# Kernel tuning notes

Hardware: AMD Instinct MI355X
Metric: run time of the kernel (lower is better)

The kernel has to match this reference:

```python
import jax, jax.numpy as jnp
import numpy as np

N_NODES = 131072
N_EDGES = 2097152
N_GRAPHS = 2048
IN_CH, HID, OUT = 12, 64, 4


def gcn_conv(x, W, b, src, dst, n_nodes):
    """PyG GCNConv: out = D^{-1/2} (A + I) D^{-1/2} (x W) + b.
    Degree computed at target nodes including self loops (edge_weight=1)."""
    h = x @ W  # [N, F_out]
    # degree with self loops: in-degree + 1
    deg = jax.ops.segment_sum(jnp.ones((src.shape[0],), x.dtype), dst,
                              num_segments=n_nodes) + 1.0
    dinv = jax.lax.rsqrt(deg)  # [N]
    norm = dinv[src] * dinv[dst]  # [E]
    # scatter-add messages from src to dst
    agg = jax.ops.segment_sum(h[src] * norm[:, None], dst, num_segments=n_nodes)
    # self-loop contribution: norm_ii = dinv[i]^2
    agg = agg + h * (dinv * dinv)[:, None]
    return agg + b


def global_mean_pool(x, batch, n_graphs):
    sums = jax.ops.segment_sum(x, batch, num_segments=n_graphs)
    cnt = jax.ops.segment_sum(jnp.ones((x.shape[0],), x.dtype), batch,
                              num_segments=n_graphs)
    return sums / jnp.maximum(cnt, 1.0)[:, None]


def setup_inputs() -> dict:
    key = jax.random.key(0)
    ks = jax.random.split(key, 9)
    x = jax.random.normal(ks[0], (N_NODES, IN_CH), dtype=jnp.float32)
    edge_index = jax.random.randint(ks[1], (2, N_EDGES), 0, N_NODES, dtype=jnp.int64)
    batch = jnp.sort(jax.random.randint(ks[2], (N_NODES,), 0, N_GRAPHS, dtype=jnp.int64))
    def glorot(k, shape):
        lim = np.sqrt(6.0 / (shape[0] + shape[1]))
        return jax.random.uniform(k, shape, jnp.float32, -lim, lim)
    return {
        "x": x,
        "edge_index": edge_index,
        "batch": batch,
        "W1": glorot(ks[3], (IN_CH, HID)),
        "b1": jnp.zeros((HID,), jnp.float32),
        "W2": glorot(ks[4], (HID, HID)),
        "b2": jnp.zeros((HID,), jnp.float32),
        "Wfc": glorot(ks[5], (HID, OUT)),
        "bfc": jnp.zeros((OUT,), jnp.float32),
    }


def reference(x, edge_index, batch, W1, b1, W2, b2, Wfc, bfc):
    src, dst = edge_index[0], edge_index[1]
    h = jax.nn.relu(gcn_conv(x, W1, b1, src, dst, N_NODES))
    h = jax.nn.relu(gcn_conv(h, W2, b2, src, dst, N_NODES))
    g = global_mean_pool(h, batch, N_GRAPHS)  # [n_graphs, HID]
    return jax.nn.sigmoid(g @ Wfc + bfc)  # [n_graphs, OUT]
```

## Files before the change

kernel.cpp:

```cpp
#include <hip/hip_runtime.h>
#include <hip/hip_bf16.h>


#define N_NODES 131072
#define N_EDGES 2097152
#define N_GRAPHS 2048
#define IN_CH 12
#define HID 64
#define OUT_CH 4
#define NBUCK 512
#define CHUNK 8192
#define STRIDE 4608
#define CSR_STRIDE 5120
#define CAP 5120

typedef float f32x2 __attribute__((ext_vector_type(2)));

__device__ __forceinline__ unsigned short f2bf(float f) {
    unsigned u = __float_as_uint(f);
    return (unsigned short)((u + 0x7fffu + ((u >> 16) & 1u)) >> 16);
}
__device__ __forceinline__ unsigned pack2bf(float lo, float hi) {
    return (unsigned)f2bf(lo) | ((unsigned)f2bf(hi) << 16);
}
__device__ __forceinline__ float bflo(unsigned v) { return __uint_as_float(v << 16); }
__device__ __forceinline__ float bfhi(unsigned v) { return __uint_as_float(v & 0xFFFF0000u); }

__global__ __launch_bounds__(1024, 4)
void bucket_kernel(const int* __restrict__ src, const int* __restrict__ dst,
                   int* __restrict__ bucket_count, int* __restrict__ staged) {
    __shared__ int hist[NBUCK];
    __shared__ int lscan[NBUCK];
    __shared__ int gbase[NBUCK];
    __shared__ int cursor[NBUCK];
    __shared__ int sorted[CHUNK];
    int tid = threadIdx.x;
    int base = blockIdx.x * CHUNK;
    if (tid < NBUCK) { hist[tid] = 0; cursor[tid] = 0; }
    __syncthreads();
    int d8[8], s8[8];
#pragma unroll
    for (int k = 0; k < 8; k++) {
        int i = base + k * 1024 + tid;
        d8[k] = dst[i];
        s8[k] = src[i];
        atomicAdd(&hist[d8[k] >> 8], 1);
    }
    __syncthreads();
    if (tid < NBUCK) lscan[tid] = hist[tid];
    __syncthreads();
    for (int off = 1; off < NBUCK; off <<= 1) {
        int u = (tid < NBUCK && tid >= off) ? lscan[tid - off] : 0;
        __syncthreads();
        if (tid < NBUCK) lscan[tid] += u;
        __syncthreads();
    }
    if (tid < NBUCK) gbase[tid] = atomicAdd(&bucket_count[tid], hist[tid]);
    __syncthreads();
#pragma unroll
    for (int k = 0; k < 8; k++) {
        int b = d8[k] >> 8;
        int start = lscan[b] - hist[b];
        int p = start + atomicAdd(&cursor[b], 1);
        sorted[p] = ((d8[k] & 255) << 17) | s8[k];
    }
    __syncthreads();
    int wid = tid >> 6, lane = tid & 63;
    int g16 = lane >> 4, k16 = lane & 15;
    for (int b0 = wid * 4; b0 < NBUCK; b0 += 64) {
        int b = b0 + g16;
        int cb = hist[b];
        int lbase = lscan[b] - cb;
        int gb = b * STRIDE + gbase[b];
        for (int k = k16; k < cb; k += 16) staged[gb + k] = sorted[lbase + k];
    }
}

__global__ void build_kernel(const int* __restrict__ bucket_count, const int* __restrict__ staged,
                             int2* __restrict__ rowbounds, float* __restrict__ dinv,
                             int* __restrict__ csr, const float* __restrict__ x,
                             unsigned short* __restrict__ xb) {
    __shared__ int sl[STRIDE];
    __shared__ int image[CAP];
    __shared__ int cnt[256];
    __shared__ int scn[256];
    __shared__ int loff[256];
    __shared__ int cursor[256];
    __shared__ int totalS;
    int b = blockIdx.x;
    int tid = threadIdx.x;
    int count = bucket_count[b];
    const int* st = staged + b * STRIDE;
    cnt[tid] = 0;
    cursor[tid] = 0;
    for (int i = tid; i < count; i += 256) sl[i] = st[i];
    __syncthreads();
    for (int i = tid; i < count; i += 256) atomicAdd(&cnt[(sl[i] >> 17) & 255], 1);
    __syncthreads();
    int deg = cnt[tid];
    int degp = (deg + 3) & ~3;
    scn[tid] = degp;
    __syncthreads();
    for (int off = 1; off < 256; off <<= 1) {
        int u = (tid >= off) ? scn[tid - off] : 0;
        __syncthreads();
        scn[tid] += u;
        __syncthreads();
    }
    int lo = scn[tid] - degp;
    loff[tid] = lo;
    int nbase = (b << 8) + tid;
    int gb = b * CSR_STRIDE;
    rowbounds[nbase] = make_int2(gb + lo, gb + lo + degp);
    float dv = rsqrtf((float)deg + 1.0f);
    dinv[nbase] = dv;
    if (tid == 255) totalS = lo + degp;
    {
        const float* xp = x + nbase * IN_CH;
        unsigned o[8];
#pragma unroll
        for (int k = 0; k < 6; k++) o[k] = pack2bf(dv * xp[2 * k], dv * xp[2 * k + 1]);
        o[6] = 0; o[7] = 0;
        uint4* dstp = (uint4*)(xb + nbase * 16);
        dstp[0] = make_uint4(o[0], o[1], o[2], o[3]);
        dstp[1] = make_uint4(o[4], o[5], o[6], o[7]);
    }
    if (b == 0 && tid < 2)
        ((uint4*)(xb + (size_t)N_NODES * 16))[tid] = make_uint4(0, 0, 0, 0);
    __syncthreads();
    for (int i = tid; i < count; i += 256) {
        int rec = sl[i];
        int s = rec & 0x1FFFF;
        int dq = (rec >> 17) & 255;
        int p = loff[dq] + atomicAdd(&cursor[dq], 1);
        int val = s << 6;
        if (p < CAP) image[p] = val;
        else csr[gb + p] = val;
    }
    __syncthreads();
    int padval = N_NODES << 6;
    for (int p = loff[tid] + deg; p < loff[tid] + degp; p++) {
        if (p < CAP) image[p] = padval;
        else csr[gb + p] = padval;
    }
    __syncthreads();
    int lim = totalS < CAP ? totalS : CAP;
    int* dstp = csr + gb;
    for (int i = tid; i < lim; i += 256) dstp[i] = image[i];
}

__global__ void agg_x_kernel(const int2* __restrict__ rowbounds, const int* __restrict__ csr,
                             const float* __restrict__ dinv,
                             const unsigned short* __restrict__ xb, float* __restrict__ aggx) {
    int tid = threadIdx.x;
    int w = tid >> 6, lane = tid & 63, sub = lane >> 1, p = lane & 1;
    int qoff = 8 * p;
    int node = (blockIdx.x * 4 + w) * 32 + sub;
    int2 rb = rowbounds[node];
    float dn = dinv[node];
    f32x2 a0[4] = {{0, 0}, {0, 0}, {0, 0}, {0, 0}};
    f32x2 a1[4] = {{0, 0}, {0, 0}, {0, 0}, {0, 0}};
    f32x2 a2[4] = {{0, 0}, {0, 0}, {0, 0}, {0, 0}};
    f32x2 a3[4] = {{0, 0}, {0, 0}, {0, 0}, {0, 0}};
    for (int j = rb.x; j < rb.y; j += 4) {
        int4 e = *(const int4*)(csr + j);
        uint4 u0 = *(const uint4*)(xb + (e.x >> 2) + qoff);
        uint4 u1 = *(const uint4*)(xb + (e.y >> 2) + qoff);
        uint4 u2 = *(const uint4*)(xb + (e.z >> 2) + qoff);
        uint4 u3 = *(const uint4*)(xb + (e.w >> 2) + qoff);
        a0[0] += (f32x2){bflo(u0.x), bfhi(u0.x)};
        a0[1] += (f32x2){bflo(u0.y), bfhi(u0.y)};
        a0[2] += (f32x2){bflo(u0.z), bfhi(u0.z)};
        a0[3] += (f32x2){bflo(u0.w), bfhi(u0.w)};
        a1[0] += (f32x2){bflo(u1.x), bfhi(u1.x)};
        a1[1] += (f32x2){bflo(u1.y), bfhi(u1.y)};
        a1[2] += (f32x2){bflo(u1.z), bfhi(u1.z)};
        a1[3] += (f32x2){bflo(u1.w), bfhi(u1.w)};
        a2[0] += (f32x2){bflo(u2.x), bfhi(u2.x)};
        a2[1] += (f32x2){bflo(u2.y), bfhi(u2.y)};
        a2[2] += (f32x2){bflo(u2.z), bfhi(u2.z)};
        a2[3] += (f32x2){bflo(u2.w), bfhi(u2.w)};
        a3[0] += (f32x2){bflo(u3.x), bfhi(u3.x)};
        a3[1] += (f32x2){bflo(u3.y), bfhi(u3.y)};
        a3[2] += (f32x2){bflo(u3.z), bfhi(u3.z)};
        a3[3] += (f32x2){bflo(u3.w), bfhi(u3.w)};
    }
    uint4 su = *(const uint4*)(xb + node * 16 + qoff);
    a0[0] += (f32x2){bflo(su.x), bfhi(su.x)};
    a0[1] += (f32x2){bflo(su.y), bfhi(su.y)};
    a0[2] += (f32x2){bflo(su.z), bfhi(su.z)};
    a0[3] += (f32x2){bflo(su.w), bfhi(su.w)};
    f32x2 nd = {dn, dn};
    f32x2 s0 = nd * ((a0[0] + a1[0]) + (a2[0] + a3[0]));
    f32x2 s1 = nd * ((a0[1] + a1[1]) + (a2[1] + a3[1]));
    f32x2 s2 = nd * ((a0[2] + a1[2]) + (a2[2] + a3[2]));
    f32x2 s3 = nd * ((a0[3] + a1[3]) + (a2[3] + a3[3]));
    float4 o0 = make_float4(s0[0], s0[1], s1[0], s1[1]);
    float4 o1 = make_float4(s2[0], s2[1], s3[0], s3[1]);
    *(float4*)(aggx + node * 16 + qoff) = o0;
    *(float4*)(aggx + node * 16 + qoff + 4) = o1;
}

__global__ void w1w2_kernel(const float* __restrict__ aggx, const float* __restrict__ W1,
                            const float* __restrict__ b1, const float* __restrict__ W2,
                            const float* __restrict__ dinv, unsigned int* __restrict__ hout) {
    __shared__ float sW1[IN_CH * HID];
    __shared__ float sW2[HID * HID];
    __shared__ float sA[64 * 17];
    __shared__ float sh1t[HID * 65];
    int tid = threadIdx.x;
    for (int i = tid; i < IN_CH * HID; i += 256) sW1[i] = W1[i];
    for (int i = tid; i < HID * HID; i += 256) sW2[i] = W2[i];
    int node0 = blockIdx.x * 64;
    {
        float4 v = *(const float4*)(aggx + node0 * 16 + tid * 4);
        int n = tid >> 2, part = (tid & 3) * 4;
        sA[n * 17 + part + 0] = v.x;
        sA[n * 17 + part + 1] = v.y;
        sA[n * 17 + part + 2] = v.z;
        sA[n * 17 + part + 3] = v.w;
    }
    __syncthreads();
    int w = tid >> 6, c = tid & 63;
    float bc = b1[c];
#pragma unroll
    for (int it = 0; it < 4; it++) {
        int n0 = w * 16 + it * 4;
        float a0 = bc, a1 = bc, a2 = bc, a3 = bc;
#pragma unroll
        for (int k = 0; k < IN_CH; k++) {
            float wv = sW1[k * HID + c];
            a0 += sA[(n0 + 0) * 17 + k] * wv;
            a1 += sA[(n0 + 1) * 17 + k] * wv;
            a2 += sA[(n0 + 2) * 17 + k] * wv;
            a3 += sA[(n0 + 3) * 17 + k] * wv;
        }
        float4 o = make_float4(fmaxf(a0, 0.0f), fmaxf(a1, 0.0f),
                               fmaxf(a2, 0.0f), fmaxf(a3, 0.0f));
        *(float4*)&sh1t[c * 65 + n0] = o;
    }
    __syncthreads();
    int nq = tid >> 4, c4 = (tid & 15) * 4;
    float4 a0 = {0, 0, 0, 0}, a1 = {0, 0, 0, 0}, a2 = {0, 0, 0, 0}, a3 = {0, 0, 0, 0};
#pragma unroll 4
    for (int k = 0; k < HID; k++) {
        float4 wv = *(const float4*)&sW2[k * HID + c4];
        float4 hv = *(const float4*)&sh1t[k * 65 + nq * 4];
        a0.x += hv.x * wv.x; a0.y += hv.x * wv.y; a0.z += hv.x * wv.z; a0.w += hv.x * wv.w;
        a1.x += hv.y * wv.x; a1.y += hv.y * wv.y; a1.z += hv.y * wv.z; a1.w += hv.y * wv.w;
        a2.x += hv.z * wv.x; a2.y += hv.z * wv.y; a2.z += hv.z * wv.z; a2.w += hv.z * wv.w;
        a3.x += hv.w * wv.x; a3.y += hv.w * wv.y; a3.z += hv.w * wv.z; a3.w += hv.w * wv.w;
    }
    int nb = node0 + nq * 4;
    float dv0 = dinv[nb + 0], dv1 = dinv[nb + 1], dv2 = dinv[nb + 2], dv3 = dinv[nb + 3];
    unsigned int p0 = (unsigned int)__builtin_amdgcn_cvt_pk_fp8_f32(dv0 * a0.x, dv0 * a0.y, 0, false);
    p0 = (unsigned int)__builtin_amdgcn_cvt_pk_fp8_f32(dv0 * a0.z, dv0 * a0.w, (int)p0, true);
    unsigned int p1 = (unsigned int)__builtin_amdgcn_cvt_pk_fp8_f32(dv1 * a1.x, dv1 * a1.y, 0, false);
    p1 = (unsigned int)__builtin_amdgcn_cvt_pk_fp8_f32(dv1 * a1.z, dv1 * a1.w, (int)p1, true);
    unsigned int p2 = (unsigned int)__builtin_amdgcn_cvt_pk_fp8_f32(dv2 * a2.x, dv2 * a2.y, 0, false);
    p2 = (unsigned int)__builtin_amdgcn_cvt_pk_fp8_f32(dv2 * a2.z, dv2 * a2.w, (int)p2, true);
    unsigned int p3 = (unsigned int)__builtin_amdgcn_cvt_pk_fp8_f32(dv3 * a3.x, dv3 * a3.y, 0, false);
    p3 = (unsigned int)__builtin_amdgcn_cvt_pk_fp8_f32(dv3 * a3.z, dv3 * a3.w, (int)p3, true);
    int cl = c4 >> 2;
    hout[(nb + 0) * 16 + cl] = p0;
    hout[(nb + 1) * 16 + cl] = p1;
    hout[(nb + 2) * 16 + cl] = p2;
    hout[(nb + 3) * 16 + cl] = p3;
    if (blockIdx.x == 0 && tid < 16)
        hout[(size_t)N_NODES * 16 + tid] = 0;
}

__device__ __forceinline__ void add_fp8(f32x2* a, uint2 u) {
    a[0] += __builtin_amdgcn_cvt_pk_f32_fp8((int)u.x, false);
    a[1] += __builtin_amdgcn_cvt_pk_f32_fp8((int)u.x, true);
    a[2] += __builtin_amdgcn_cvt_pk_f32_fp8((int)u.y, false);
    a[3] += __builtin_amdgcn_cvt_pk_f32_fp8((int)u.y, true);
}

__device__ __forceinline__ void agg_body(int beg, int end, const int* __restrict__ csr,
                                         const unsigned char* __restrict__ h,
                                         int qoff, float* r) {
    f32x2 a0[4] = {{0, 0}, {0, 0}, {0, 0}, {0, 0}};
    f32x2 a1[4] = {{0, 0}, {0, 0}, {0, 0}, {0, 0}};
    f32x2 a2[4] = {{0, 0}, {0, 0}, {0, 0}, {0, 0}};
    f32x2 a3[4] = {{0, 0}, {0, 0}, {0, 0}, {0, 0}};
    int j = beg;
    for (; j + 8 <= end; j += 8) {
        int4 ea = *(const int4*)(csr + j);
        int4 eb = *(const int4*)(csr + j + 4);
        uint2 u0 = *(const uint2*)(h + ea.x + qoff);
        uint2 u1 = *(const uint2*)(h + ea.y + qoff);
        uint2 u2 = *(const uint2*)(h + ea.z + qoff);
        uint2 u3 = *(const uint2*)(h + ea.w + qoff);
        uint2 u4 = *(const uint2*)(h + eb.x + qoff);
        uint2 u5 = *(const uint2*)(h + eb.y + qoff);
        uint2 u6 = *(const uint2*)(h + eb.z + qoff);
        uint2 u7 = *(const uint2*)(h + eb.w + qoff);
        add_fp8(a0, u0); add_fp8(a1, u1); add_fp8(a2, u2); add_fp8(a3, u3);
        add_fp8(a0, u4); add_fp8(a1, u5); add_fp8(a2, u6); add_fp8(a3, u7);
    }
    if (j < end) {
        int4 ea = *(const int4*)(csr + j);
        uint2 u0 = *(const uint2*)(h + ea.x + qoff);
        uint2 u1 = *(const uint2*)(h + ea.y + qoff);
        uint2 u2 = *(const uint2*)(h + ea.z + qoff);
        uint2 u3 = *(const uint2*)(h + ea.w + qoff);
        add_fp8(a0, u0); add_fp8(a1, u1); add_fp8(a2, u2); add_fp8(a3, u3);
    }
#pragma unroll
    for (int k = 0; k < 4; k++) {
        f32x2 s = (a0[k] + a1[k]) + (a2[k] + a3[k]);
        r[2 * k] = s[0];
        r[2 * k + 1] = s[1];
    }
}

__global__ void agg_pool_kernel(const int2* __restrict__ rowbounds, const int* __restrict__ csr,
                                const float* __restrict__ dinv,
                                const unsigned char* __restrict__ h,
                                const float* __restrict__ b, const int* __restrict__ batch,
                                float* __restrict__ pool, float* __restrict__ gcnt) {
    __shared__ float red[32][HID];
    __shared__ int gids[32];
    int tid = threadIdx.x;
    int w = tid >> 6, lane = tid & 63, sub = lane >> 3, q = lane & 7;
    int qoff = 8 * q;
    int node = (blockIdx.x * 4 + w) * 8 + sub;
    int2 rb = rowbounds[node];
    float dn = dinv[node];
    float r[8];
    agg_body(rb.x, rb.y, csr, h, qoff, r);
    uint2 su = *(const uint2*)(h + node * HID + qoff);
    f32x2 s0 = __builtin_amdgcn_cvt_pk_f32_fp8((int)su.x, false);
    f32x2 s1 = __builtin_amdgcn_cvt_pk_f32_fp8((int)su.x, true);
    f32x2 s2 = __builtin_amdgcn_cvt_pk_f32_fp8((int)su.y, false);
    f32x2 s3 = __builtin_amdgcn_cvt_pk_f32_fp8((int)su.y, true);
    float4 b0 = *(const float4*)&b[qoff];
    float4 b1 = *(const float4*)&b[qoff + 4];
    float4 v0, v1;
    v0.x = fmaxf(dn * (r[0] + s0[0]) + b0.x, 0.0f);
    v0.y = fmaxf(dn * (r[1] + s0[1]) + b0.y, 0.0f);
    v0.z = fmaxf(dn * (r[2] + s1[0]) + b0.z, 0.0f);
    v0.w = fmaxf(dn * (r[3] + s1[1]) + b0.w, 0.0f);
    v1.x = fmaxf(dn * (r[4] + s2[0]) + b1.x, 0.0f);
    v1.y = fmaxf(dn * (r[5] + s2[1]) + b1.y, 0.0f);
    v1.z = fmaxf(dn * (r[6] + s3[0]) + b1.z, 0.0f);
    v1.w = fmaxf(dn * (r[7] + s3[1]) + b1.w, 0.0f);
    int nl = w * 8 + sub;
    *(float4*)&red[nl][qoff] = v0;
    *(float4*)&red[nl][qoff + 4] = v1;
    if (q == 0) gids[nl] = batch[node];
    __syncthreads();
    if (tid < 64) {
        int c = tid;
        float acc = 0.0f;
        int cur = gids[0], cnt = 0;
        for (int n = 0; n < 32; n++) {
            int g = gids[n];
            if (g != cur) {
                atomicAdd(&pool[cur * HID + c], acc);
                if (c == 0) atomicAdd(&gcnt[cur], (float)cnt);
                acc = 0.0f; cnt = 0; cur = g;
            }
            acc += red[n][c];
            cnt++;
        }
        atomicAdd(&pool[cur * HID + c], acc);
        if (c == 0) atomicAdd(&gcnt[cur], (float)cnt);
    }
}

__global__ void final_kernel(const float* __restrict__ pool, const float* __restrict__ gcnt,
                             const float* __restrict__ Wfc, const float* __restrict__ bfc,
                             float* __restrict__ out) {
    int idx = blockIdx.x * 256 + threadIdx.x;
    if (idx >= N_GRAPHS * OUT_CH) return;
    int g = idx >> 2, o = idx & 3;
    float inv = 1.0f / fmaxf(gcnt[g], 1.0f);
    float acc = bfc[o];
#pragma unroll
    for (int k = 0; k < HID; k++) acc += pool[g * HID + k] * inv * Wfc[k * OUT_CH + o];
    out[idx] = 1.0f / (1.0f + expf(-acc));
}

extern "C" void kernel_launch(void* const* d_in, const int* in_sizes, int n_in,
                              void* d_out, int out_size, void* d_ws, size_t ws_size,
                              hipStream_t stream) {
    const float* x   = (const float*)d_in[0];
    const int* eidx  = (const int*)d_in[1];
    const int* batch = (const int*)d_in[2];
    const float* W1  = (const float*)d_in[3];
    const float* b1  = (const float*)d_in[4];
    const float* W2  = (const float*)d_in[5];
    const float* b2  = (const float*)d_in[6];
    const float* Wfc = (const float*)d_in[7];
    const float* bfc = (const float*)d_in[8];
    float* out = (float*)d_out;

    const int* src = eidx;
    const int* dst = eidx + N_EDGES;

    unsigned char* hB = (unsigned char*)d_ws;
    int*   csr    = (int*)(hB + (size_t)(N_NODES + 1) * HID);
    int*   staged = csr + (size_t)NBUCK * CSR_STRIDE;
    float* dinv   = (float*)(staged + (size_t)NBUCK * STRIDE);
    int2*  rowbounds = (int2*)(dinv + N_NODES);
    int*   bucket_count = (int*)(rowbounds + N_NODES);
    float* pool   = (float*)(bucket_count + NBUCK);
    float* gcnt   = pool + N_GRAPHS * HID;
    unsigned short* xb = (unsigned short*)(gcnt + N_GRAPHS);
    float* aggx   = (float*)(xb + (size_t)(N_NODES + 1) * 16);

    hipMemsetAsync(bucket_count, 0, (size_t)NBUCK * 4, stream);
    hipMemsetAsync(pool, 0, (size_t)(N_GRAPHS * HID + N_GRAPHS) * 4, stream);

    bucket_kernel<<<N_EDGES / CHUNK, 1024, 0, stream>>>(src, dst, bucket_count, staged);
    build_kernel<<<NBUCK, 256, 0, stream>>>(bucket_count, staged, rowbounds, dinv, csr, x, xb);

    agg_x_kernel<<<N_NODES / 128, 256, 0, stream>>>(rowbounds, csr, dinv, xb, aggx);
    w1w2_kernel<<<N_NODES / 64, 256, 0, stream>>>(aggx, W1, b1, W2, dinv, (unsigned int*)hB);

    agg_pool_kernel<<<N_NODES / 32, 256, 0, stream>>>(rowbounds, csr, dinv, hB, b2, batch,
                                                      pool, gcnt);

    final_kernel<<<(N_GRAPHS * OUT_CH + 255) / 256, 256, 0, stream>>>(pool, gcnt, Wfc, bfc, out);
}
```

Measured before the change: 190.3 us.

## Replace bucketed two-pass CSR build with atomic count, reserve, and place

Replaces the shared-memory bucket sort and per-bucket build with three kernels. The first counts in-degrees with global atomics and records each edge's rank in a byte array. The second scans degrees per block and reserves CSR space with a global atomic cursor. The third scatters each edge directly to its slot. This removes the staging buffer and the LDS sort, but adds global atomics on random addresses, scattered CSR writes, and a rank stored in 8 bits that wraps if any node has in-degree of 256 or more. Row placement now depends on the order in which blocks reach the atomic cursor, so edge order inside a row is also nondeterministic.

```diff
diff --git a/kernel.cpp b/kernel.cpp
--- a/kernel.cpp
+++ b/kernel.cpp
@@ -8,11 +8,7 @@
 #define IN_CH 12
 #define HID 64
 #define OUT_CH 4
-#define NBUCK 512
-#define CHUNK 8192
-#define STRIDE 4608
-#define CSR_STRIDE 5120
-#define CAP 5120
+#define CSR_CAP 2560000
 
 typedef float f32x2 __attribute__((ext_vector_type(2)));
 
@@ -26,79 +22,28 @@
 __device__ __forceinline__ float bflo(unsigned v) { return __uint_as_float(v << 16); }
 __device__ __forceinline__ float bfhi(unsigned v) { return __uint_as_float(v & 0xFFFF0000u); }
 
-__global__ __launch_bounds__(1024, 4)
-void bucket_kernel(const int* __restrict__ src, const int* __restrict__ dst,
-                   int* __restrict__ bucket_count, int* __restrict__ staged) {
-    __shared__ int hist[NBUCK];
-    __shared__ int lscan[NBUCK];
-    __shared__ int gbase[NBUCK];
-    __shared__ int cursor[NBUCK];
-    __shared__ int sorted[CHUNK];
-    int tid = threadIdx.x;
-    int base = blockIdx.x * CHUNK;
-    if (tid < NBUCK) { hist[tid] = 0; cursor[tid] = 0; }
-    __syncthreads();
-    int d8[8], s8[8];
-#pragma unroll
-    for (int k = 0; k < 8; k++) {
-        int i = base + k * 1024 + tid;
-        d8[k] = dst[i];
-        s8[k] = src[i];
-        atomicAdd(&hist[d8[k] >> 8], 1);
-    }
-    __syncthreads();
-    if (tid < NBUCK) lscan[tid] = hist[tid];
-    __syncthreads();
-    for (int off = 1; off < NBUCK; off <<= 1) {
-        int u = (tid < NBUCK && tid >= off) ? lscan[tid - off] : 0;
-        __syncthreads();
-        if (tid < NBUCK) lscan[tid] += u;
-        __syncthreads();
-    }
-    if (tid < NBUCK) gbase[tid] = atomicAdd(&bucket_count[tid], hist[tid]);
-    __syncthreads();
-#pragma unroll
-    for (int k = 0; k < 8; k++) {
-        int b = d8[k] >> 8;
-        int start = lscan[b] - hist[b];
-        int p = start + atomicAdd(&cursor[b], 1);
-        sorted[p] = ((d8[k] & 255) << 17) | s8[k];
-    }
-    __syncthreads();
-    int wid = tid >> 6, lane = tid & 63;
-    int g16 = lane >> 4, k16 = lane & 15;
-    for (int b0 = wid * 4; b0 < NBUCK; b0 += 64) {
-        int b = b0 + g16;
-        int cb = hist[b];
-        int lbase = lscan[b] - cb;
-        int gb = b * STRIDE + gbase[b];
-        for (int k = k16; k < cb; k += 16) staged[gb + k] = sorted[lbase + k];
-    }
-}
-
-__global__ void build_kernel(const int* __restrict__ bucket_count, const int* __restrict__ staged,
-                             int2* __restrict__ rowbounds, float* __restrict__ dinv,
-                             int* __restrict__ csr, const float* __restrict__ x,
-                             unsigned short* __restrict__ xb) {
-    __shared__ int sl[STRIDE];
-    __shared__ int image[CAP];
-    __shared__ int cnt[256];
+__global__ void count_kernel(const int* __restrict__ dst, int* __restrict__ deg,
+                             unsigned char* __restrict__ rank) {
+    int i = (blockIdx.x * 256 + threadIdx.x) * 4;
+    int4 d = *(const int4*)(dst + i);
+    unsigned r0 = (unsigned)atomicAdd(&deg[d.x], 1);
+    unsigned r1 = (unsigned)atomicAdd(&deg[d.y], 1);
+    unsigned r2 = (unsigned)atomicAdd(&deg[d.z], 1);
+    unsigned r3 = (unsigned)atomicAdd(&deg[d.w], 1);
+    *(uchar4*)(rank + i) = make_uchar4((unsigned char)r0, (unsigned char)r1,
+                                       (unsigned char)r2, (unsigned char)r3);
+}
+
+__global__ void reserve_kernel(const int* __restrict__ deg, int* __restrict__ gcur,
+                               int2* __restrict__ rowbounds, float* __restrict__ dinv,
+                               int* __restrict__ csr, const float* __restrict__ x,
+                               unsigned short* __restrict__ xb) {
     __shared__ int scn[256];
-    __shared__ int loff[256];
-    __shared__ int cursor[256];
-    __shared__ int totalS;
-    int b = blockIdx.x;
-    int tid = threadIdx.x;
-    int count = bucket_count[b];
-    const int* st = staged + b * STRIDE;
-    cnt[tid] = 0;
-    cursor[tid] = 0;
-    for (int i = tid; i < count; i += 256) sl[i] = st[i];
-    __syncthreads();
-    for (int i = tid; i < count; i += 256) atomicAdd(&cnt[(sl[i] >> 17) & 255], 1);
-    __syncthreads();
-    int deg = cnt[tid];
-    int degp = (deg + 3) & ~3;
+    __shared__ int sbase;
+    int b = blockIdx.x, tid = threadIdx.x;
+    int n = b * 256 + tid;
+    int dg = deg[n];
+    int degp = (dg + 3) & ~3;
     scn[tid] = degp;
     __syncthreads();
     for (int off = 1; off < 256; off <<= 1) {
@@ -107,46 +52,40 @@
         scn[tid] += u;
         __syncthreads();
     }
-    int lo = scn[tid] - degp;
-    loff[tid] = lo;
-    int nbase = (b << 8) + tid;
-    int gb = b * CSR_STRIDE;
-    rowbounds[nbase] = make_int2(gb + lo, gb + lo + degp);
-    float dv = rsqrtf((float)deg + 1.0f);
-    dinv[nbase] = dv;
-    if (tid == 255) totalS = lo + degp;
+    if (tid == 255) sbase = atomicAdd(gcur, scn[255]);
+    __syncthreads();
+    int lo = sbase + scn[tid] - degp;
+    rowbounds[n] = make_int2(lo, lo + degp);
+    float dv = rsqrtf((float)dg + 1.0f);
+    dinv[n] = dv;
+    int padval = N_NODES << 6;
+    for (int p = lo + dg; p < lo + degp; p++) csr[p] = padval;
     {
-        const float* xp = x + nbase * IN_CH;
+        const float* xp = x + n * IN_CH;
         unsigned o[8];
 #pragma unroll
         for (int k = 0; k < 6; k++) o[k] = pack2bf(dv * xp[2 * k], dv * xp[2 * k + 1]);
         o[6] = 0; o[7] = 0;
-        uint4* dstp = (uint4*)(xb + nbase * 16);
+        uint4* dstp = (uint4*)(xb + n * 16);
         dstp[0] = make_uint4(o[0], o[1], o[2], o[3]);
         dstp[1] = make_uint4(o[4], o[5], o[6], o[7]);
     }
     if (b == 0 && tid < 2)
         ((uint4*)(xb + (size_t)N_NODES * 16))[tid] = make_uint4(0, 0, 0, 0);
-    __syncthreads();
-    for (int i = tid; i < count; i += 256) {
-        int rec = sl[i];
-        int s = rec & 0x1FFFF;
-        int dq = (rec >> 17) & 255;
-        int p = loff[dq] + atomicAdd(&cursor[dq], 1);
-        int val = s << 6;
-        if (p < CAP) image[p] = val;
-        else csr[gb + p] = val;
-    }
-    __syncthreads();
-    int padval = N_NODES << 6;
-    for (int p = loff[tid] + deg; p < loff[tid] + degp; p++) {
-        if (p < CAP) image[p] = padval;
-        else csr[gb + p] = padval;
-    }
-    __syncthreads();
-    int lim = totalS < CAP ? totalS : CAP;
-    int* dstp = csr + gb;
-    for (int i = tid; i < lim; i += 256) dstp[i] = image[i];
+}
+
+__global__ void place_kernel(const int* __restrict__ src, const int* __restrict__ dst,
+                             const unsigned char* __restrict__ rank,
+                             const int2* __restrict__ rowbounds, int* __restrict__ csr) {
+    int i = (blockIdx.x * 256 + threadIdx.x) * 4;
+    int4 s = *(const int4*)(src + i);
+    int4 d = *(const int4*)(dst + i);
+    uchar4 r = *(const uchar4*)(rank + i);
+    const int* rs = (const int*)rowbounds;
+    csr[rs[2 * d.x] + r.x] = s.x << 6;
+    csr[rs[2 * d.y] + r.y] = s.y << 6;
+    csr[rs[2 * d.z] + r.z] = s.z << 6;
+    csr[rs[2 * d.w] + r.w] = s.w << 6;
 }
 
 __global__ void agg_x_kernel(const int2* __restrict__ rowbounds, const int* __restrict__ csr,
@@ -401,21 +340,22 @@
     const int* dst = eidx + N_EDGES;
 
     unsigned char* hB = (unsigned char*)d_ws;
-    int*   csr    = (int*)(hB + (size_t)(N_NODES + 1) * HID);
-    int*   staged = csr + (size_t)NBUCK * CSR_STRIDE;
-    float* dinv   = (float*)(staged + (size_t)NBUCK * STRIDE);
+    int*   csr  = (int*)(hB + (size_t)(N_NODES + 1) * HID);
+    float* dinv = (float*)(csr + CSR_CAP);
     int2*  rowbounds = (int2*)(dinv + N_NODES);
-    int*   bucket_count = (int*)(rowbounds + N_NODES);
-    float* pool   = (float*)(bucket_count + NBUCK);
-    float* gcnt   = pool + N_GRAPHS * HID;
-    unsigned short* xb = (unsigned short*)(gcnt + N_GRAPHS);
-    float* aggx   = (float*)(xb + (size_t)(N_NODES + 1) * 16);
-
-    hipMemsetAsync(bucket_count, 0, (size_t)NBUCK * 4, stream);
-    hipMemsetAsync(pool, 0, (size_t)(N_GRAPHS * HID + N_GRAPHS) * 4, stream);
-
-    bucket_kernel<<<N_EDGES / CHUNK, 1024, 0, stream>>>(src, dst, bucket_count, staged);
-    build_kernel<<<NBUCK, 256, 0, stream>>>(bucket_count, staged, rowbounds, dinv, csr, x, xb);
+    unsigned short* xb = (unsigned short*)(rowbounds + N_NODES);
+    float* aggx = (float*)(xb + (size_t)(N_NODES + 1) * 16);
+    unsigned char* rank = (unsigned char*)(aggx + (size_t)N_NODES * 16);
+    int*   deg  = (int*)(rank + N_EDGES);
+    float* pool = (float*)(deg + N_NODES);
+    float* gcnt = pool + N_GRAPHS * HID;
+    int*   gcur = (int*)(gcnt + N_GRAPHS);
+
+    hipMemsetAsync(deg, 0, (size_t)(N_NODES + N_GRAPHS * HID + N_GRAPHS + 4) * 4, stream);
+
+    count_kernel<<<N_EDGES / 1024, 256, 0, stream>>>(dst, deg, rank);
+    reserve_kernel<<<N_NODES / 256, 256, 0, stream>>>(deg, gcur, rowbounds, dinv, csr, x, xb);
+    place_kernel<<<N_EDGES / 1024, 256, 0, stream>>>(src, dst, rank, rowbounds, csr);
 
     agg_x_kernel<<<N_NODES / 128, 256, 0, stream>>>(rowbounds, csr, dinv, xb, aggx);
     w1w2_kernel<<<N_NODES / 64, 256, 0, stream>>>(aggx, W1, b1, W2, dinv, (unsigned int*)hB);
```

Measured after the change: 290.9 us. 1.53x slower.

## Fuse layer-1 aggregation into W1/W2 kernel and widen layer-2 gather to 16 bytes

Applied to the files above, without the earlier changes.

Folds the first-layer neighbour aggregation into the dense W1/W2 kernel, so each node's row is split across two lanes that combine their halves with a shuffle. This removes the fp32 aggx intermediate round trip and one kernel launch. The pooled aggregation kernel now gives each lane 16 fp8 channels via 16-byte loads, uses 4 lanes per node and 64 nodes per block, which halves the pool atomics per node. The two memsets are merged into one, which relies on bucket_count and pool being contiguous in the workspace. The trade-offs are fewer threads in flight for the gather phases and more registers per lane.

```diff
diff --git a/kernel.cpp b/kernel.cpp
--- a/kernel.cpp
+++ b/kernel.cpp
@@ -149,61 +149,10 @@
     for (int i = tid; i < lim; i += 256) dstp[i] = image[i];
 }
 
-__global__ void agg_x_kernel(const int2* __restrict__ rowbounds, const int* __restrict__ csr,
-                             const float* __restrict__ dinv,
-                             const unsigned short* __restrict__ xb, float* __restrict__ aggx) {
-    int tid = threadIdx.x;
-    int w = tid >> 6, lane = tid & 63, sub = lane >> 1, p = lane & 1;
-    int qoff = 8 * p;
-    int node = (blockIdx.x * 4 + w) * 32 + sub;
-    int2 rb = rowbounds[node];
-    float dn = dinv[node];
-    f32x2 a0[4] = {{0, 0}, {0, 0}, {0, 0}, {0, 0}};
-    f32x2 a1[4] = {{0, 0}, {0, 0}, {0, 0}, {0, 0}};
-    f32x2 a2[4] = {{0, 0}, {0, 0}, {0, 0}, {0, 0}};
-    f32x2 a3[4] = {{0, 0}, {0, 0}, {0, 0}, {0, 0}};
-    for (int j = rb.x; j < rb.y; j += 4) {
-        int4 e = *(const int4*)(csr + j);
-        uint4 u0 = *(const uint4*)(xb + (e.x >> 2) + qoff);
-        uint4 u1 = *(const uint4*)(xb + (e.y >> 2) + qoff);
-        uint4 u2 = *(const uint4*)(xb + (e.z >> 2) + qoff);
-        uint4 u3 = *(const uint4*)(xb + (e.w >> 2) + qoff);
-        a0[0] += (f32x2){bflo(u0.x), bfhi(u0.x)};
-        a0[1] += (f32x2){bflo(u0.y), bfhi(u0.y)};
-        a0[2] += (f32x2){bflo(u0.z), bfhi(u0.z)};
-        a0[3] += (f32x2){bflo(u0.w), bfhi(u0.w)};
-        a1[0] += (f32x2){bflo(u1.x), bfhi(u1.x)};
-        a1[1] += (f32x2){bflo(u1.y), bfhi(u1.y)};
-        a1[2] += (f32x2){bflo(u1.z), bfhi(u1.z)};
-        a1[3] += (f32x2){bflo(u1.w), bfhi(u1.w)};
-        a2[0] += (f32x2){bflo(u2.x), bfhi(u2.x)};
-        a2[1] += (f32x2){bflo(u2.y), bfhi(u2.y)};
-        a2[2] += (f32x2){bflo(u2.z), bfhi(u2.z)};
-        a2[3] += (f32x2){bflo(u2.w), bfhi(u2.w)};
-        a3[0] += (f32x2){bflo(u3.x), bfhi(u3.x)};
-        a3[1] += (f32x2){bflo(u3.y), bfhi(u3.y)};
-        a3[2] += (f32x2){bflo(u3.z), bfhi(u3.z)};
-        a3[3] += (f32x2){bflo(u3.w), bfhi(u3.w)};
-    }
-    uint4 su = *(const uint4*)(xb + node * 16 + qoff);
-    a0[0] += (f32x2){bflo(su.x), bfhi(su.x)};
-    a0[1] += (f32x2){bflo(su.y), bfhi(su.y)};
-    a0[2] += (f32x2){bflo(su.z), bfhi(su.z)};
-    a0[3] += (f32x2){bflo(su.w), bfhi(su.w)};
-    f32x2 nd = {dn, dn};
-    f32x2 s0 = nd * ((a0[0] + a1[0]) + (a2[0] + a3[0]));
-    f32x2 s1 = nd * ((a0[1] + a1[1]) + (a2[1] + a3[1]));
-    f32x2 s2 = nd * ((a0[2] + a1[2]) + (a2[2] + a3[2]));
-    f32x2 s3 = nd * ((a0[3] + a1[3]) + (a2[3] + a3[3]));
-    float4 o0 = make_float4(s0[0], s0[1], s1[0], s1[1]);
-    float4 o1 = make_float4(s2[0], s2[1], s3[0], s3[1]);
-    *(float4*)(aggx + node * 16 + qoff) = o0;
-    *(float4*)(aggx + node * 16 + qoff + 4) = o1;
-}
-
-__global__ void w1w2_kernel(const float* __restrict__ aggx, const float* __restrict__ W1,
-                            const float* __restrict__ b1, const float* __restrict__ W2,
-                            const float* __restrict__ dinv, unsigned int* __restrict__ hout) {
+__global__ void w1w2_kernel(const int2* __restrict__ rowbounds, const int* __restrict__ csr,
+                            const float* __restrict__ dinv, const unsigned short* __restrict__ xb,
+                            const float* __restrict__ W1, const float* __restrict__ b1,
+                            const float* __restrict__ W2, unsigned int* __restrict__ hout) {
     __shared__ float sW1[IN_CH * HID];
     __shared__ float sW2[HID * HID];
     __shared__ float sA[64 * 17];
@@ -213,12 +162,62 @@
     for (int i = tid; i < HID * HID; i += 256) sW2[i] = W2[i];
     int node0 = blockIdx.x * 64;
     {
-        float4 v = *(const float4*)(aggx + node0 * 16 + tid * 4);
-        int n = tid >> 2, part = (tid & 3) * 4;
-        sA[n * 17 + part + 0] = v.x;
-        sA[n * 17 + part + 1] = v.y;
-        sA[n * 17 + part + 2] = v.z;
-        sA[n * 17 + part + 3] = v.w;
+        int nl = tid >> 2;
+        int node = node0 + nl;
+        int p = tid & 1, qoff = 8 * p;
+        int2 rb = rowbounds[node];
+        int len = rb.y - rb.x;
+        int hlen = (len >> 3) << 2;
+        int beg = (tid & 2) ? rb.x + hlen : rb.x;
+        int end = (tid & 2) ? rb.y : rb.x + hlen;
+        f32x2 a0[4] = {{0, 0}, {0, 0}, {0, 0}, {0, 0}};
+        f32x2 a1[4] = {{0, 0}, {0, 0}, {0, 0}, {0, 0}};
+        f32x2 a2[4] = {{0, 0}, {0, 0}, {0, 0}, {0, 0}};
+        f32x2 a3[4] = {{0, 0}, {0, 0}, {0, 0}, {0, 0}};
+        for (int j = beg; j < end; j += 4) {
+            int4 e = *(const int4*)(csr + j);
+            uint4 u0 = *(const uint4*)(xb + (e.x >> 2) + qoff);
+            uint4 u1 = *(const uint4*)(xb + (e.y >> 2) + qoff);
+            uint4 u2 = *(const uint4*)(xb + (e.z >> 2) + qoff);
+            uint4 u3 = *(const uint4*)(xb + (e.w >> 2) + qoff);
+            a0[0] += (f32x2){bflo(u0.x), bfhi(u0.x)};
+            a0[1] += (f32x2){bflo(u0.y), bfhi(u0.y)};
+            a0[2] += (f32x2){bflo(u0.z), bfhi(u0.z)};
+            a0[3] += (f32x2){bflo(u0.w), bfhi(u0.w)};
+            a1[0] += (f32x2){bflo(u1.x), bfhi(u1.x)};
+            a1[1] += (f32x2){bflo(u1.y), bfhi(u1.y)};
+            a1[2] += (f32x2){bflo(u1.z), bfhi(u1.z)};
+            a1[3] += (f32x2){bflo(u1.w), bfhi(u1.w)};
+            a2[0] += (f32x2){bflo(u2.x), bfhi(u2.x)};
+            a2[1] += (f32x2){bflo(u2.y), bfhi(u2.y)};
+            a2[2] += (f32x2){bflo(u2.z), bfhi(u2.z)};
+            a2[3] += (f32x2){bflo(u2.w), bfhi(u2.w)};
+            a3[0] += (f32x2){bflo(u3.x), bfhi(u3.x)};
+            a3[1] += (f32x2){bflo(u3.y), bfhi(u3.y)};
+            a3[2] += (f32x2){bflo(u3.z), bfhi(u3.z)};
+            a3[3] += (f32x2){bflo(u3.w), bfhi(u3.w)};
+        }
+        f32x2 s0 = (a0[0] + a1[0]) + (a2[0] + a3[0]);
+        f32x2 s1 = (a0[1] + a1[1]) + (a2[1] + a3[1]);
+        f32x2 s2 = (a0[2] + a1[2]) + (a2[2] + a3[2]);
+        f32x2 s3 = (a0[3] + a1[3]) + (a2[3] + a3[3]);
+        s0[0] += __shfl_xor(s0[0], 2); s0[1] += __shfl_xor(s0[1], 2);
+        s1[0] += __shfl_xor(s1[0], 2); s1[1] += __shfl_xor(s1[1], 2);
+        s2[0] += __shfl_xor(s2[0], 2); s2[1] += __shfl_xor(s2[1], 2);
+        s3[0] += __shfl_xor(s3[0], 2); s3[1] += __shfl_xor(s3[1], 2);
+        if (!(tid & 2)) {
+            uint4 su = *(const uint4*)(xb + node * 16 + qoff);
+            s0 += (f32x2){bflo(su.x), bfhi(su.x)};
+            s1 += (f32x2){bflo(su.y), bfhi(su.y)};
+            s2 += (f32x2){bflo(su.z), bfhi(su.z)};
+            s3 += (f32x2){bflo(su.w), bfhi(su.w)};
+            float dn = dinv[node];
+            float* dp = &sA[nl * 17 + qoff];
+            dp[0] = dn * s0[0]; dp[1] = dn * s0[1];
+            dp[2] = dn * s1[0]; dp[3] = dn * s1[1];
+            dp[4] = dn * s2[0]; dp[5] = dn * s2[1];
+            dp[6] = dn * s3[0]; dp[7] = dn * s3[1];
+        }
     }
     __syncthreads();
     int w = tid >> 6, c = tid & 63;
@@ -270,46 +269,48 @@
         hout[(size_t)N_NODES * 16 + tid] = 0;
 }
 
-__device__ __forceinline__ void add_fp8(f32x2* a, uint2 u) {
+__device__ __forceinline__ void add_fp8q(f32x2* a, uint4 u) {
     a[0] += __builtin_amdgcn_cvt_pk_f32_fp8((int)u.x, false);
     a[1] += __builtin_amdgcn_cvt_pk_f32_fp8((int)u.x, true);
     a[2] += __builtin_amdgcn_cvt_pk_f32_fp8((int)u.y, false);
     a[3] += __builtin_amdgcn_cvt_pk_f32_fp8((int)u.y, true);
-}
-
-__device__ __forceinline__ void agg_body(int beg, int end, const int* __restrict__ csr,
-                                         const unsigned char* __restrict__ h,
-                                         int qoff, float* r) {
-    f32x2 a0[4] = {{0, 0}, {0, 0}, {0, 0}, {0, 0}};
-    f32x2 a1[4] = {{0, 0}, {0, 0}, {0, 0}, {0, 0}};
-    f32x2 a2[4] = {{0, 0}, {0, 0}, {0, 0}, {0, 0}};
-    f32x2 a3[4] = {{0, 0}, {0, 0}, {0, 0}, {0, 0}};
+    a[4] += __builtin_amdgcn_cvt_pk_f32_fp8((int)u.z, false);
+    a[5] += __builtin_amdgcn_cvt_pk_f32_fp8((int)u.z, true);
+    a[6] += __builtin_amdgcn_cvt_pk_f32_fp8((int)u.w, false);
+    a[7] += __builtin_amdgcn_cvt_pk_f32_fp8((int)u.w, true);
+}
+
+__device__ __forceinline__ void agg_body16(int beg, int end, const int* __restrict__ csr,
+                                           const unsigned char* __restrict__ h,
+                                           int qoff, float* r) {
+    f32x2 a0[8] = {{0, 0}, {0, 0}, {0, 0}, {0, 0}, {0, 0}, {0, 0}, {0, 0}, {0, 0}};
+    f32x2 a1[8] = {{0, 0}, {0, 0}, {0, 0}, {0, 0}, {0, 0}, {0, 0}, {0, 0}, {0, 0}};
     int j = beg;
     for (; j + 8 <= end; j += 8) {
         int4 ea = *(const int4*)(csr + j);
         int4 eb = *(const int4*)(csr + j + 4);
-        uint2 u0 = *(const uint2*)(h + ea.x + qoff);
-        uint2 u1 = *(const uint2*)(h + ea.y + qoff);
-        uint2 u2 = *(const uint2*)(h + ea.z + qoff);
-        uint2 u3 = *(const uint2*)(h + ea.w + qoff);
-        uint2 u4 = *(const uint2*)(h + eb.x + qoff);
-        uint2 u5 = *(const uint2*)(h + eb.y + qoff);
-        uint2 u6 = *(const uint2*)(h + eb.z + qoff);
-        uint2 u7 = *(const uint2*)(h + eb.w + qoff);
-        add_fp8(a0, u0); add_fp8(a1, u1); add_fp8(a2, u2); add_fp8(a3, u3);
-        add_fp8(a0, u4); add_fp8(a1, u5); add_fp8(a2, u6); add_fp8(a3, u7);
+        uint4 u0 = *(const uint4*)(h + ea.x + qoff);
+        uint4 u1 = *(const uint4*)(h + ea.y + qoff);
+        uint4 u2 = *(const uint4*)(h + ea.z + qoff);
+        uint4 u3 = *(const uint4*)(h + ea.w + qoff);
+        uint4 u4 = *(const uint4*)(h + eb.x + qoff);
+        uint4 u5 = *(const uint4*)(h + eb.y + qoff);
+        uint4 u6 = *(const uint4*)(h + eb.z + qoff);
+        uint4 u7 = *(const uint4*)(h + eb.w + qoff);
+        add_fp8q(a0, u0); add_fp8q(a1, u1); add_fp8q(a0, u2); add_fp8q(a1, u3);
+        add_fp8q(a0, u4); add_fp8q(a1, u5); add_fp8q(a0, u6); add_fp8q(a1, u7);
     }
     if (j < end) {
         int4 ea = *(const int4*)(csr + j);
-        uint2 u0 = *(const uint2*)(h + ea.x + qoff);
-        uint2 u1 = *(const uint2*)(h + ea.y + qoff);
-        uint2 u2 = *(const uint2*)(h + ea.z + qoff);
-        uint2 u3 = *(const uint2*)(h + ea.w + qoff);
-        add_fp8(a0, u0); add_fp8(a1, u1); add_fp8(a2, u2); add_fp8(a3, u3);
-    }
-#pragma unroll
-    for (int k = 0; k < 4; k++) {
-        f32x2 s = (a0[k] + a1[k]) + (a2[k] + a3[k]);
+        uint4 u0 = *(const uint4*)(h + ea.x + qoff);
+        uint4 u1 = *(const uint4*)(h + ea.y + qoff);
+        uint4 u2 = *(const uint4*)(h + ea.z + qoff);
+        uint4 u3 = *(const uint4*)(h + ea.w + qoff);
+        add_fp8q(a0, u0); add_fp8q(a1, u1); add_fp8q(a0, u2); add_fp8q(a1, u3);
+    }
+#pragma unroll
+    for (int k = 0; k < 8; k++) {
+        f32x2 s = a0[k] + a1[k];
         r[2 * k] = s[0];
         r[2 * k + 1] = s[1];
     }
@@ -320,42 +321,43 @@
                                 const unsigned char* __restrict__ h,
                                 const float* __restrict__ b, const int* __restrict__ batch,
                                 float* __restrict__ pool, float* __restrict__ gcnt) {
-    __shared__ float red[32][HID];
-    __shared__ int gids[32];
+    __shared__ float red[64][HID + 4];
+    __shared__ int gids[64];
     int tid = threadIdx.x;
-    int w = tid >> 6, lane = tid & 63, sub = lane >> 3, q = lane & 7;
-    int qoff = 8 * q;
-    int node = (blockIdx.x * 4 + w) * 8 + sub;
+    int w = tid >> 6, lane = tid & 63, sub = lane >> 2, q = lane & 3;
+    int qoff = 16 * q;
+    int node = (blockIdx.x * 4 + w) * 16 + sub;
     int2 rb = rowbounds[node];
     float dn = dinv[node];
-    float r[8];
-    agg_body(rb.x, rb.y, csr, h, qoff, r);
-    uint2 su = *(const uint2*)(h + node * HID + qoff);
-    f32x2 s0 = __builtin_amdgcn_cvt_pk_f32_fp8((int)su.x, false);
-    f32x2 s1 = __builtin_amdgcn_cvt_pk_f32_fp8((int)su.x, true);
-    f32x2 s2 = __builtin_amdgcn_cvt_pk_f32_fp8((int)su.y, false);
-    f32x2 s3 = __builtin_amdgcn_cvt_pk_f32_fp8((int)su.y, true);
-    float4 b0 = *(const float4*)&b[qoff];
-    float4 b1 = *(const float4*)&b[qoff + 4];
-    float4 v0, v1;
-    v0.x = fmaxf(dn * (r[0] + s0[0]) + b0.x, 0.0f);
-    v0.y = fmaxf(dn * (r[1] + s0[1]) + b0.y, 0.0f);
-    v0.z = fmaxf(dn * (r[2] + s1[0]) + b0.z, 0.0f);
-    v0.w = fmaxf(dn * (r[3] + s1[1]) + b0.w, 0.0f);
-    v1.x = fmaxf(dn * (r[4] + s2[0]) + b1.x, 0.0f);
-    v1.y = fmaxf(dn * (r[5] + s2[1]) + b1.y, 0.0f);
-    v1.z = fmaxf(dn * (r[6] + s3[0]) + b1.z, 0.0f);
-    v1.w = fmaxf(dn * (r[7] + s3[1]) + b1.w, 0.0f);
-    int nl = w * 8 + sub;
-    *(float4*)&red[nl][qoff] = v0;
-    *(float4*)&red[nl][qoff + 4] = v1;
+    float r[16];
+    agg_body16(rb.x, rb.y, csr, h, qoff, r);
+    uint4 su = *(const uint4*)(h + node * HID + qoff);
+    f32x2 s[8];
+    s[0] = __builtin_amdgcn_cvt_pk_f32_fp8((int)su.x, false);
+    s[1] = __builtin_amdgcn_cvt_pk_f32_fp8((int)su.x, true);
+    s[2] = __builtin_amdgcn_cvt_pk_f32_fp8((int)su.y, false);
+    s[3] = __builtin_amdgcn_cvt_pk_f32_fp8((int)su.y, true);
+    s[4] = __builtin_amdgcn_cvt_pk_f32_fp8((int)su.z, false);
+    s[5] = __builtin_amdgcn_cvt_pk_f32_fp8((int)su.z, true);
+    s[6] = __builtin_amdgcn_cvt_pk_f32_fp8((int)su.w, false);
+    s[7] = __builtin_amdgcn_cvt_pk_f32_fp8((int)su.w, true);
+    int nl = w * 16 + sub;
+    float* rp = &red[nl][qoff];
+#pragma unroll
+    for (int k = 0; k < 4; k++) {
+        float4 bv = *(const float4*)&b[qoff + 4 * k];
+        rp[4 * k + 0] = fmaxf(dn * (r[4 * k + 0] + s[2 * k][0]) + bv.x, 0.0f);
+        rp[4 * k + 1] = fmaxf(dn * (r[4 * k + 1] + s[2 * k][1]) + bv.y, 0.0f);
+        rp[4 * k + 2] = fmaxf(dn * (r[4 * k + 2] + s[2 * k + 1][0]) + bv.z, 0.0f);
+        rp[4 * k + 3] = fmaxf(dn * (r[4 * k + 3] + s[2 * k + 1][1]) + bv.w, 0.0f);
+    }
     if (q == 0) gids[nl] = batch[node];
     __syncthreads();
     if (tid < 64) {
         int c = tid;
         float acc = 0.0f;
         int cur = gids[0], cnt = 0;
-        for (int n = 0; n < 32; n++) {
+        for (int n = 0; n < 64; n++) {
             int g = gids[n];
             if (g != cur) {
                 atomicAdd(&pool[cur * HID + c], acc);
@@ -409,18 +411,17 @@
     float* pool   = (float*)(bucket_count + NBUCK);
     float* gcnt   = pool + N_GRAPHS * HID;
     unsigned short* xb = (unsigned short*)(gcnt + N_GRAPHS);
-    float* aggx   = (float*)(xb + (size_t)(N_NODES + 1) * 16);
-
-    hipMemsetAsync(bucket_count, 0, (size_t)NBUCK * 4, stream);
-    hipMemsetAsync(pool, 0, (size_t)(N_GRAPHS * HID + N_GRAPHS) * 4, stream);
+
+    hipMemsetAsync(bucket_count, 0,
+                   (size_t)(NBUCK + N_GRAPHS * HID + N_GRAPHS) * 4, stream);
 
     bucket_kernel<<<N_EDGES / CHUNK, 1024, 0, stream>>>(src, dst, bucket_count, staged);
     build_kernel<<<NBUCK, 256, 0, stream>>>(bucket_count, staged, rowbounds, dinv, csr, x, xb);
 
-    agg_x_kernel<<<N_NODES / 128, 256, 0, stream>>>(rowbounds, csr, dinv, xb, aggx);
-    w1w2_kernel<<<N_NODES / 64, 256, 0, stream>>>(aggx, W1, b1, W2, dinv, (unsigned int*)hB);
-
-    agg_pool_kernel<<<N_NODES / 32, 256, 0, stream>>>(rowbounds, csr, dinv, hB, b2, batch,
+    w1w2_kernel<<<N_NODES / 64, 256, 0, stream>>>(rowbounds, csr, dinv, xb, W1, b1, W2,
+                                                  (unsigned int*)hB);
+
+    agg_pool_kernel<<<N_NODES / 64, 256, 0, stream>>>(rowbounds, csr, dinv, hB, b2, batch,
                                                       pool, gcnt);
 
     final_kernel<<<(N_GRAPHS * OUT_CH + 255) / 256, 256, 0, stream>>>(pool, gcnt, Wfc, bfc, out);
```

Result: faster. 185.7 us (-2.4%).
